# Performance work log

Measured on AMD Instinct MI355X. Metric: run time of the kernel, lower is better.

## Reference

```python
import jax, jax.numpy as jnp
import numpy as np
import math

B, A, IN_C, OUT_C = 64, 128, 128, 64

def _l2norm(x, eps=1e-12):
    # matches F.normalize(dim=1) on 2D input: x / max(||x||_2, eps) along last dim
    n = jnp.sqrt(jnp.sum(x * x, axis=-1, keepdims=True))
    return x / jnp.maximum(n, eps)

def setup_inputs() -> dict:
    key = jax.random.key(0)
    ks = jax.random.split(key, 7)
    s = 1.0 / math.sqrt(IN_C)
    return {
        "features": jax.random.normal(ks[0], (B, IN_C, A), dtype=jnp.float32),
        "Wq": jax.random.uniform(ks[1], (OUT_C, IN_C), jnp.float32, -s, s),
        "bq": jax.random.uniform(ks[2], (OUT_C,), jnp.float32, -s, s),
        "Wk": jax.random.uniform(ks[3], (OUT_C, IN_C), jnp.float32, -s, s),
        "bk": jax.random.uniform(ks[4], (OUT_C,), jnp.float32, -s, s),
        "Wv": jax.random.uniform(ks[5], (OUT_C, IN_C), jnp.float32, -s, s),
        "bv": jax.random.uniform(ks[6], (OUT_C,), jnp.float32, -s, s),
    }

def reference(features, Wq, bq, Wk, bk, Wv, bv):
    b = features.shape[0]
    f = jnp.transpose(features, (0, 2, 1))          # (b, a, in_c)
    a = f.shape[1]
    q = f @ Wq.T + bq                               # (b, a, d)
    k = f @ Wk.T + bk
    v = f @ Wv.T + bv
    d = q.shape[-1]
    qf = q.reshape(-1, d)                           # (N, d), N = b*a
    kf = k.reshape(-1, d)
    vf = v.reshape(-1, d)
    att = jax.nn.softmax(qf @ kf.T / math.sqrt(d), axis=1)  # (N, N)
    qkv = att @ vf                                  # (N, d)
    qkv_n = _l2norm(qkv).reshape(b, a, d)
    v_n = _l2norm(vf).reshape(b, a, d)
    # sim_s[i,j] = (1/a) * sum_t v_n[i,t] . qkv_n[j,t]  (diagonal-trace over 'a')
    sim_s = jnp.einsum('bad,cad->bc', v_n, qkv_n) / a
    return sim_s
```

## Files before the change

kernel.cpp:

```cpp
#include <hip/hip_runtime.h>
#include <hip/hip_bf16.h>

#define NROW 8192
#define INC  128
#define OUTC 64

#define QSCALE 0.18033688011112042f

typedef __bf16 bf16x8 __attribute__((ext_vector_type(8)));
typedef __bf16 bf16x4 __attribute__((ext_vector_type(4)));
typedef short  s16x4  __attribute__((ext_vector_type(4)));
typedef float  f32x4  __attribute__((ext_vector_type(4)));

static __device__ __forceinline__ f32x4 mfma16(bf16x8 a, bf16x8 b, f32x4 c) {
    return __builtin_amdgcn_mfma_f32_16x16x32_bf16(a, b, c, 0, 0, 0);
}
static __device__ __forceinline__ f32x4 mfma1k(s16x4 a, s16x4 b, f32x4 c) {
    return __builtin_amdgcn_mfma_f32_16x16x16bf16_1k(a, b, c, 0, 0, 0);
}

static __device__ __forceinline__ bf16x8 cvt8(float4 lo, float4 hi) {
    bf16x8 r;
    r[0] = (__bf16)lo.x; r[1] = (__bf16)lo.y; r[2] = (__bf16)lo.z; r[3] = (__bf16)lo.w;
    r[4] = (__bf16)hi.x; r[5] = (__bf16)hi.y; r[6] = (__bf16)hi.z; r[7] = (__bf16)hi.w;
    return r;
}

__global__ __launch_bounds__(256) void proj_kernel(
    const float* __restrict__ feat,
    const float* __restrict__ Wq, const float* __restrict__ bq,
    const float* __restrict__ Wk, const float* __restrict__ bk,
    const float* __restrict__ Wv, const float* __restrict__ bv,
    __hip_bfloat16* __restrict__ qbf, __hip_bfloat16* __restrict__ kbf,
    __hip_bfloat16* __restrict__ vbf, __hip_bfloat16* __restrict__ vnb)
{
    __shared__ float slab[32 * 132];
    __shared__ float vbuf[32 * 66];
    __shared__ float invb[32];

    const int blk = blockIdx.x;
    const int mat = blk >> 8;
    const int b   = (blk >> 2) & 63;
    const int a0  = (blk & 3) * 32;
    const int r0  = b * 128 + a0;
    const float* fb = feat + (size_t)b * INC * 128;

    for (int i = threadIdx.x; i < 32 * 128; i += 256) {
        int c = i >> 5, a = i & 31;
        slab[a * 132 + c] = fb[c * 128 + a0 + a];
    }
    __syncthreads();

    const int w    = threadIdx.x >> 6;
    const int lane = threadIdx.x & 63;
    const int l16  = lane & 15;
    const int quad = lane >> 4;
    const int n0   = w * 16;

    const float* W    = (mat == 0) ? Wq : (mat == 1) ? Wk : Wv;
    const float* bias = (mat == 0) ? bq : (mat == 1) ? bk : bv;

    f32x4 acc[2] = {{0.f,0.f,0.f,0.f},{0.f,0.f,0.f,0.f}};
    #pragma unroll
    for (int kc = 0; kc < 4; ++kc) {
        const int k0 = kc * 32 + quad * 8;
        const float* wr = W + (n0 + l16) * INC + k0;
        bf16x8 bfr = cvt8(*(const float4*)wr, *(const float4*)(wr + 4));
        #pragma unroll
        for (int u = 0; u < 2; ++u) {
            const float* ar = slab + (u * 16 + l16) * 132 + k0;
            bf16x8 afr = cvt8(*(const float4*)ar, *(const float4*)(ar + 4));
            acc[u] = mfma16(afr, bfr, acc[u]);
        }
    }
    const float bl = bias[n0 + l16];
    const float sc = (mat == 0) ? QSCALE : 1.0f;

    if (mat < 2) {
        __hip_bfloat16* dst = mat ? kbf : qbf;
        #pragma unroll
        for (int u = 0; u < 2; ++u) {
            const int base = ((((r0 >> 4) + u) * 4 + w) << 8) + l16;
            #pragma unroll
            for (int r = 0; r < 4; ++r)
                dst[base + (quad * 4 + r) * 16] = __float2bfloat16((acc[u][r] + bl) * sc);
        }
    } else {
        #pragma unroll
        for (int u = 0; u < 2; ++u)
            #pragma unroll
            for (int r = 0; r < 4; ++r)
                vbuf[(u * 16 + quad * 4 + r) * 66 + n0 + l16] = acc[u][r] + bl;
        __syncthreads();
        const int rl = threadIdx.x >> 3;
        const int jj = threadIdx.x & 7;
        float ss = 0.f;
        #pragma unroll
        for (int i = 0; i < 8; ++i) {
            float x = vbuf[rl * 66 + jj * 8 + i];
            ss += x * x;
        }
        ss += __shfl_xor(ss, 1, 64);
        ss += __shfl_xor(ss, 2, 64);
        ss += __shfl_xor(ss, 4, 64);
        if (jj == 0) invb[rl] = rsqrtf(fmaxf(ss, 1e-24f));
        __syncthreads();
        float inv = invb[rl];
        bf16x8 vp;
        #pragma unroll
        for (int i = 0; i < 8; ++i)
            vp[i] = (__bf16)(vbuf[rl * 66 + jj * 8 + i] * inv);
        *(bf16x8*)(vnb + (size_t)(r0 + rl) * 64 + jj * 8) = vp;
        const int tl = threadIdx.x & 15;
        const int n  = (threadIdx.x >> 4) & 3;
        const int s_ = threadIdx.x >> 6;
        bf16x8 pack;
        #pragma unroll
        for (int j = 0; j < 8; ++j) {
            int key = s_ * 8 + j;
            pack[j] = (__bf16)(vbuf[key * 66 + n * 16 + tl] * invb[key]);
        }
        const int base = ((((r0 >> 4) + (s_ >> 1)) * 4 + n) << 8) + tl * 16 + (s_ & 1) * 8;
        *(bf16x8*)(vbf + base) = pack;
    }
}

__global__ __launch_bounds__(256) void attn_kernel(
    const __hip_bfloat16* __restrict__ qbf,
    const __hip_bfloat16* __restrict__ kbf,
    const __hip_bfloat16* __restrict__ vbf,
    float* __restrict__ Opart, float* __restrict__ lpart)
{
    __shared__ float ored[2][32][65];
    __shared__ float lred[2][32];

    const int qtile = blockIdx.x >> 3;
    const int bg    = blockIdx.x & 7;
    const int w     = threadIdx.x >> 6;
    const int lane  = threadIdx.x & 63;
    const int l16   = lane & 15;
    const int quad  = lane >> 4;
    const int r0    = qtile * 32;
    const int fo    = l16 * 16 + quad * 4;
    const int fo32  = l16 * 16 + (quad & 1) * 8;
    const int qh    = quad >> 1;

    bf16x8 qf32[2][2];
    #pragma unroll
    for (int u = 0; u < 2; ++u)
        #pragma unroll
        for (int p = 0; p < 2; ++p)
            qf32[u][p] = *(const bf16x8*)(qbf +
                ((((r0 >> 4) + u) * 4 + p * 2 + qh) << 8) + fo32);

    f32x4 of[2][4];
    float lp[2] = {0.f, 0.f};
    #pragma unroll
    for (int u = 0; u < 2; ++u)
        #pragma unroll
        for (int n = 0; n < 4; ++n)
            of[u][n] = (f32x4){0.f, 0.f, 0.f, 0.f};

    const int ck0 = bg * 64 + w * 16;
    bf16x8 kfA[2][2], kfB[2][2];
    #pragma unroll
    for (int h = 0; h < 2; ++h)
        #pragma unroll
        for (int p = 0; p < 2; ++p)
            kfA[h][p] = *(const bf16x8*)(kbf +
                (((ck0 + h) * 4 + p * 2 + qh) << 8) + fo32);

    #pragma unroll 1
    for (int it = 0; it < 8; it += 2) {
        #pragma unroll
        for (int st = 0; st < 2; ++st) {
            const int ck = ck0 + (it + st) * 2;
            bf16x8 (&kf)[2][2] = (st == 0) ? kfA : kfB;
            bf16x8 (&kn)[2][2] = (st == 0) ? kfB : kfA;
            s16x4 vf[4][2];
            #pragma unroll
            for (int n = 0; n < 4; ++n)
                #pragma unroll
                for (int h = 0; h < 2; ++h)
                    vf[n][h] = *(const s16x4*)(vbf + (((ck + h) * 4 + n) << 8) + fo);
            const int cnext = (it + st + 1 < 8) ? ck + 2 : ck;
            #pragma unroll
            for (int h = 0; h < 2; ++h)
                #pragma unroll
                for (int p = 0; p < 2; ++p)
                    kn[h][p] = *(const bf16x8*)(kbf +
                        (((cnext + h) * 4 + p * 2 + qh) << 8) + fo32);

            const f32x4 zero = (f32x4){0.f, 0.f, 0.f, 0.f};
            #pragma unroll
            for (int u = 0; u < 2; ++u) {
                f32x4 s0 = mfma16(kf[0][0], qf32[u][0], zero);
                s0       = mfma16(kf[0][1], qf32[u][1], s0);
                f32x4 s1 = mfma16(kf[1][0], qf32[u][0], zero);
                s1       = mfma16(kf[1][1], qf32[u][1], s1);
                union { bf16x4 v; s16x4 s; } pf0, pf1;
                #pragma unroll
                for (int r = 0; r < 4; ++r) {
                    float p0 = __builtin_amdgcn_exp2f(s0[r]);
                    float p1 = __builtin_amdgcn_exp2f(s1[r]);
                    lp[u] += p0 + p1;
                    pf0.v[r] = (__bf16)p0;
                    pf1.v[r] = (__bf16)p1;
                }
                #pragma unroll
                for (int n = 0; n < 4; ++n) {
                    of[u][n] = mfma1k(pf0.s, vf[n][0], of[u][n]);
                    of[u][n] = mfma1k(pf1.s, vf[n][1], of[u][n]);
                }
            }
        }
    }

    #pragma unroll
    for (int u = 0; u < 2; ++u) {
        float v = lp[u];
        v += __shfl_xor(v, 16, 64);
        v += __shfl_xor(v, 32, 64);
        lp[u] = v;
    }

    if (w >= 2) {
        #pragma unroll
        for (int u = 0; u < 2; ++u)
            #pragma unroll
            for (int n = 0; n < 4; ++n)
                #pragma unroll
                for (int r = 0; r < 4; ++r)
                    ored[w - 2][u * 16 + quad * 4 + r][n * 16 + l16] = of[u][n][r];
        if (quad == 0) {
            lred[w - 2][l16]      = lp[0];
            lred[w - 2][16 + l16] = lp[1];
        }
    }
    __syncthreads();
    if (w < 2) {
        #pragma unroll
        for (int u = 0; u < 2; ++u)
            #pragma unroll
            for (int n = 0; n < 4; ++n)
                #pragma unroll
                for (int r = 0; r < 4; ++r) {
                    float v = of[u][n][r] + ored[w][u * 16 + quad * 4 + r][n * 16 + l16];
                    ored[w][u * 16 + quad * 4 + r][n * 16 + l16] = v;
                }
        if (quad == 0) {
            lred[w][l16]      += lp[0];
            lred[w][16 + l16] += lp[1];
        }
    }
    __syncthreads();
    const int task = blockIdx.x;
    float* Ob = Opart + (size_t)task * 2048;
    for (int e = threadIdx.x; e < 2048; e += 256) {
        const int row = e >> 6, col = e & 63;
        Ob[e] = ored[0][row][col] + ored[1][row][col];
    }
    if (threadIdx.x < 32)
        lpart[task * 32 + threadIdx.x] = lred[0][threadIdx.x] + lred[1][threadIdx.x];
}

__global__ __launch_bounds__(256) void combine_kernel(
    const float* __restrict__ Opart, const float* __restrict__ lpart,
    __hip_bfloat16* __restrict__ qnb)
{
    const int r    = blockIdx.x * 4 + (threadIdx.x >> 6);
    const int c    = threadIdx.x & 63;
    const int tile = r >> 5, row = r & 31;
    float acc = 0.f, lsum = 0.f;
    #pragma unroll
    for (int g = 0; g < 8; ++g) {
        int task = tile * 8 + g;
        acc  += Opart[(size_t)task * 2048 + row * 64 + c];
        lsum += lpart[task * 32 + row];
    }
    float q = acc / lsum;
    float ss = q * q;
    ss += __shfl_xor(ss, 1, 64);
    ss += __shfl_xor(ss, 2, 64);
    ss += __shfl_xor(ss, 4, 64);
    ss += __shfl_xor(ss, 8, 64);
    ss += __shfl_xor(ss, 16, 64);
    ss += __shfl_xor(ss, 32, 64);
    qnb[(size_t)r * 64 + c] = __float2bfloat16(q * rsqrtf(fmaxf(ss, 1e-24f)));
}

__global__ __launch_bounds__(64) void sim_kernel(
    const __hip_bfloat16* __restrict__ vnb,
    const __hip_bfloat16* __restrict__ qnb,
    float* __restrict__ out)
{
    const int lane = threadIdx.x;
    const int l16  = lane & 15;
    const int quad = lane >> 4;
    const int kblk = blockIdx.x * 256;

    f32x4 acc[4][4];
    #pragma unroll
    for (int mi = 0; mi < 4; ++mi)
        #pragma unroll
        for (int ni = 0; ni < 4; ++ni)
            acc[mi][ni] = (f32x4){0.f, 0.f, 0.f, 0.f};

    #pragma unroll
    for (int ks = 0; ks < 8; ++ks) {
        const int k0 = kblk + ks * 32 + quad * 8;
        bf16x8 af[4], bfv[4];
        #pragma unroll
        for (int mi = 0; mi < 4; ++mi)
            af[mi] = *(const bf16x8*)(vnb + (size_t)(mi * 16 + l16) * 8192 + k0);
        #pragma unroll
        for (int ni = 0; ni < 4; ++ni)
            bfv[ni] = *(const bf16x8*)(qnb + (size_t)(ni * 16 + l16) * 8192 + k0);
        #pragma unroll
        for (int mi = 0; mi < 4; ++mi)
            #pragma unroll
            for (int ni = 0; ni < 4; ++ni)
                acc[mi][ni] = mfma16(af[mi], bfv[ni], acc[mi][ni]);
    }

    #pragma unroll
    for (int mi = 0; mi < 4; ++mi)
        #pragma unroll
        for (int ni = 0; ni < 4; ++ni)
            #pragma unroll
            for (int r = 0; r < 4; ++r)
                atomicAdd(&out[(mi * 16 + quad * 4 + r) * 64 + ni * 16 + l16],
                          acc[mi][ni][r] * (1.f / 128.f));
}

extern "C" void kernel_launch(void* const* d_in, const int* in_sizes, int n_in,
                              void* d_out, int out_size, void* d_ws, size_t ws_size,
                              hipStream_t stream)
{
    const float* feat = (const float*)d_in[0];
    const float* Wq   = (const float*)d_in[1];
    const float* bq   = (const float*)d_in[2];
    const float* Wk   = (const float*)d_in[3];
    const float* bk   = (const float*)d_in[4];
    const float* Wv   = (const float*)d_in[5];
    const float* bv   = (const float*)d_in[6];
    float* out = (float*)d_out;

    const size_t MB = 1u << 20;
    char* ws = (char*)d_ws;
    __hip_bfloat16* qbf = (__hip_bfloat16*)(ws);
    __hip_bfloat16* kbf = (__hip_bfloat16*)(ws + 1 * MB);
    __hip_bfloat16* vbf = (__hip_bfloat16*)(ws + 2 * MB);
    __hip_bfloat16* vnb = (__hip_bfloat16*)(ws + 3 * MB);
    float* Opart = (float*)(ws + 4 * MB);
    float* lpart = (float*)(ws + 20 * MB);
    __hip_bfloat16* qnb = (__hip_bfloat16*)(ws + 21 * MB);

    (void)hipMemsetAsync(out, 0, 64 * 64 * sizeof(float), stream);
    proj_kernel<<<768, 256, 0, stream>>>(feat, Wq, bq, Wk, bk, Wv, bv, qbf, kbf, vbf, vnb);
    attn_kernel<<<2048, 256, 0, stream>>>(qbf, kbf, vbf, Opart, lpart);
    combine_kernel<<<2048, 256, 0, stream>>>(Opart, lpart, qnb);
    sim_kernel<<<32, 64, 0, stream>>>(vnb, qnb, out);
}
```

Before: 122.5 us.

## Give each wave its own query tile and drop the in-block LDS reduction

The attention kernel now assigns each of the four waves a separate 32-row query tile over the full 64-chunk key group, instead of splitting one tile's keys across waves. This removes the shared-memory partial reduction and both barriers, lets each wave write its partial O and l straight to global memory, and cuts the grid from 2048 to 512 blocks. K/V addressing is also switched to incrementing byte pointers. Each wave now runs a longer serial loop, and the four waves in a block read the same K/V, which relies on cache reuse; fewer blocks may reduce occupancy or tail balance.

```diff
diff --git a/kernel.cpp b/kernel.cpp
--- a/kernel.cpp
+++ b/kernel.cpp
@@ -131,16 +131,13 @@
     const __hip_bfloat16* __restrict__ vbf,
     float* __restrict__ Opart, float* __restrict__ lpart)
 {
-    __shared__ float ored[2][32][65];
-    __shared__ float lred[2][32];
-
-    const int qtile = blockIdx.x >> 3;
+    const int qb    = blockIdx.x >> 3;
     const int bg    = blockIdx.x & 7;
     const int w     = threadIdx.x >> 6;
     const int lane  = threadIdx.x & 63;
     const int l16   = lane & 15;
     const int quad  = lane >> 4;
-    const int r0    = qtile * 32;
+    const int r0    = qb * 128 + w * 32;
     const int fo    = l16 * 16 + quad * 4;
     const int fo32  = l16 * 16 + (quad & 1) * 8;
     const int qh    = quad >> 1;
@@ -161,20 +158,22 @@
         for (int n = 0; n < 4; ++n)
             of[u][n] = (f32x4){0.f, 0.f, 0.f, 0.f};
 
-    const int ck0 = bg * 64 + w * 16;
+    const int ck0 = bg * 64;
+    const char* kp = (const char*)kbf + ck0 * 2048 + qh * 512 + fo32 * 2;
+    const char* vp = (const char*)vbf + ck0 * 2048 + fo * 2;
+
     bf16x8 kfA[2][2], kfB[2][2];
     #pragma unroll
     for (int h = 0; h < 2; ++h)
         #pragma unroll
         for (int p = 0; p < 2; ++p)
-            kfA[h][p] = *(const bf16x8*)(kbf +
-                (((ck0 + h) * 4 + p * 2 + qh) << 8) + fo32);
+            kfA[h][p] = *(const bf16x8*)(kp + h * 2048 + p * 1024);
+    kp += 4096;
 
     #pragma unroll 1
-    for (int it = 0; it < 8; it += 2) {
+    for (int body = 0; body < 16; ++body) {
         #pragma unroll
         for (int st = 0; st < 2; ++st) {
-            const int ck = ck0 + (it + st) * 2;
             bf16x8 (&kf)[2][2] = (st == 0) ? kfA : kfB;
             bf16x8 (&kn)[2][2] = (st == 0) ? kfB : kfA;
             s16x4 vf[4][2];
@@ -182,14 +181,14 @@
             for (int n = 0; n < 4; ++n)
                 #pragma unroll
                 for (int h = 0; h < 2; ++h)
-                    vf[n][h] = *(const s16x4*)(vbf + (((ck + h) * 4 + n) << 8) + fo);
-            const int cnext = (it + st + 1 < 8) ? ck + 2 : ck;
+                    vf[n][h] = *(const s16x4*)(vp + h * 2048 + n * 512);
             #pragma unroll
             for (int h = 0; h < 2; ++h)
                 #pragma unroll
                 for (int p = 0; p < 2; ++p)
-                    kn[h][p] = *(const bf16x8*)(kbf +
-                        (((cnext + h) * 4 + p * 2 + qh) << 8) + fo32);
+                    kn[h][p] = *(const bf16x8*)(kp + h * 2048 + p * 1024);
+            vp += 4096;
+            kp += 4096;
 
             const f32x4 zero = (f32x4){0.f, 0.f, 0.f, 0.f};
             #pragma unroll
@@ -203,7 +202,7 @@
                 for (int r = 0; r < 4; ++r) {
                     float p0 = __builtin_amdgcn_exp2f(s0[r]);
                     float p1 = __builtin_amdgcn_exp2f(s1[r]);
-                    lp[u] += p0 + p1;
+                    lp[0 + u] += p0 + p1;
                     pf0.v[r] = (__bf16)p0;
                     pf1.v[r] = (__bf16)p1;
                 }
@@ -224,44 +223,19 @@
         lp[u] = v;
     }
 
-    if (w >= 2) {
-        #pragma unroll
-        for (int u = 0; u < 2; ++u)
-            #pragma unroll
-            for (int n = 0; n < 4; ++n)
-                #pragma unroll
-                for (int r = 0; r < 4; ++r)
-                    ored[w - 2][u * 16 + quad * 4 + r][n * 16 + l16] = of[u][n][r];
-        if (quad == 0) {
-            lred[w - 2][l16]      = lp[0];
-            lred[w - 2][16 + l16] = lp[1];
-        }
-    }
-    __syncthreads();
-    if (w < 2) {
-        #pragma unroll
-        for (int u = 0; u < 2; ++u)
-            #pragma unroll
-            for (int n = 0; n < 4; ++n)
-                #pragma unroll
-                for (int r = 0; r < 4; ++r) {
-                    float v = of[u][n][r] + ored[w][u * 16 + quad * 4 + r][n * 16 + l16];
-                    ored[w][u * 16 + quad * 4 + r][n * 16 + l16] = v;
-                }
-        if (quad == 0) {
-            lred[w][l16]      += lp[0];
-            lred[w][16 + l16] += lp[1];
-        }
-    }
-    __syncthreads();
-    const int task = blockIdx.x;
+    const int task = (qb * 4 + w) * 8 + bg;
     float* Ob = Opart + (size_t)task * 2048;
-    for (int e = threadIdx.x; e < 2048; e += 256) {
-        const int row = e >> 6, col = e & 63;
-        Ob[e] = ored[0][row][col] + ored[1][row][col];
-    }
-    if (threadIdx.x < 32)
-        lpart[task * 32 + threadIdx.x] = lred[0][threadIdx.x] + lred[1][threadIdx.x];
+    #pragma unroll
+    for (int u = 0; u < 2; ++u)
+        #pragma unroll
+        for (int n = 0; n < 4; ++n)
+            #pragma unroll
+            for (int r = 0; r < 4; ++r)
+                Ob[(u * 16 + quad * 4 + r) * 64 + n * 16 + l16] = of[u][n][r];
+    if (quad == 0) {
+        lpart[task * 32 + l16]      = lp[0];
+        lpart[task * 32 + 16 + l16] = lp[1];
+    }
 }
 
 __global__ __launch_bounds__(256) void combine_kernel(
@@ -358,7 +332,7 @@
 
     (void)hipMemsetAsync(out, 0, 64 * 64 * sizeof(float), stream);
     proj_kernel<<<768, 256, 0, stream>>>(feat, Wq, bq, Wk, bk, Wv, bv, qbf, kbf, vbf, vnb);
-    attn_kernel<<<2048, 256, 0, stream>>>(qbf, kbf, vbf, Opart, lpart);
+    attn_kernel<<<512, 256, 0, stream>>>(qbf, kbf, vbf, Opart, lpart);
     combine_kernel<<<2048, 256, 0, stream>>>(Opart, lpart, qnb);
     sim_kernel<<<32, 64, 0, stream>>>(vnb, qnb, out);
 }
```

New measurement: 120.8 us. No clear change (-1.4%).
